# Kernel tuning notes

Measured on AMD Instinct MI355X. Metric: run time of the kernel, lower is better.

The kernel has to match this reference:

```python
import jax, jax.numpy as jnp
import numpy as np

B, S, D, H = 2, 2048, 1024, 16
DK = D // H


def setup_inputs() -> dict:
    key = jax.random.key(0)
    ks = jax.random.split(key, 11)
    sd = 1.0 / np.sqrt(D)  # torch Linear default init scale (uniform bound)
    def lin(k):
        kw, kb = jax.random.split(k)
        W = jax.random.uniform(kw, (D, D), jnp.float32, -sd, sd)
        b = jax.random.uniform(kb, (D,), jnp.float32, -sd, sd)
        return W, b
    Wq, bq = lin(ks[0]); Wk, bk = lin(ks[1]); Wv, bv = lin(ks[2]); Wo, bo = lin(ks[3])
    return {
        "Q": jax.random.normal(ks[4], (B, S, D), jnp.float32),
        "K": jax.random.normal(ks[5], (B, S, D), jnp.float32),
        "V": jax.random.normal(ks[6], (B, S, D), jnp.float32),
        "mask": jnp.ones((B, S), jnp.int32),
        "Wq": Wq, "bq": bq, "Wk": Wk, "bk": bk,
        "Wv": Wv, "bv": bv, "Wo": Wo, "bo": bo,
    }


def reference(Q, K, V, mask, Wq, bq, Wk, bk, Wv, bv, Wo, bo):
    b, s, _ = Q.shape
    # projections (torch Linear: x @ W.T + b), split heads -> [b, h, s, dk]
    def proj(x, W, bias):
        return (x @ W.T + bias).reshape(b, -1, H, DK).transpose(0, 2, 1, 3)
    q = proj(Q, Wq, bq)
    k = proj(K, Wk, bk)
    v = proj(V, Wv, bv)
    scores = jnp.einsum('bhqd,bhkd->bhqk', q, k) / jnp.sqrt(jnp.float32(DK))
    m = mask[:, None, None, :]  # [b,1,1,s_k]
    scores = jnp.where(m == 0, jnp.float32(-jnp.inf), scores)
    attn = jax.nn.softmax(scores, axis=-1)
    out = jnp.einsum('bhqk,bhkd->bhqd', attn, v)
    out = out.transpose(0, 2, 1, 3).reshape(b, s, H * DK)
    return out @ Wo.T + bo
```

## Files before the change

### kernel.cpp

```cpp
#include <hip/hip_runtime.h>
#include <stdint.h>

#define BB 2
#define HH 16
#define SS 2048
#define DKK 64
#define DD 1024
#define TT (BB * SS)

typedef __attribute__((ext_vector_type(8))) short bf16x8;
typedef __attribute__((ext_vector_type(4))) float f32x4;
typedef __attribute__((ext_vector_type(16))) float f32x16;

static __device__ __forceinline__ unsigned short f2bf(float f) {
  union { float f; uint32_t u; } c; c.f = f;
  return (unsigned short)((c.u + 0x7FFFu + ((c.u >> 16) & 1u)) >> 16);
}

static __device__ __forceinline__ f32x4 zero4() {
  f32x4 z; z[0] = 0.f; z[1] = 0.f; z[2] = 0.f; z[3] = 0.f; return z;
}
static __device__ __forceinline__ f32x16 zero16() {
  f32x16 z;
#pragma unroll
  for (int i = 0; i < 16; ++i) z[i] = 0.f;
  return z;
}

static __device__ __forceinline__ uint32_t cvt_pk_bf16(float lo, float hi) {
  uint32_t r;
  asm("v_cvt_pk_bf16_f32 %0, %1, %2" : "=v"(r) : "v"(lo), "v"(hi));
  return r;
}

static __device__ __forceinline__ uint32_t xswap_u32(uint32_t v) {
  return (uint32_t)__shfl_xor((int)v, 32);
}
static __device__ __forceinline__ float xhalf_sum(float x) {
  return x + __shfl_xor(x, 32);
}

static __device__ __forceinline__ void gload_lds16(const void* g, void* l) {
  __builtin_amdgcn_global_load_lds(
      (const __attribute__((address_space(1))) void*)g,
      (__attribute__((address_space(3))) void*)l, 16, 0, 0);
}

static __device__ __forceinline__ int swz(int row, int col) {
  return ((((col >> 3) ^ row) & 7) << 3) | (col & 7);
}

struct CvtArgs {
  const float* src[4];
  unsigned short* dst[4];
  int n4[4];
};

__global__ __launch_bounds__(256) void cvt_all(CvtArgs a) {
  const int id = blockIdx.y;
  const float4* s = (const float4*)a.src[id];
  ushort4* d = (ushort4*)a.dst[id];
  const int n4 = a.n4[id];
  for (int i = blockIdx.x * blockDim.x + threadIdx.x; i < n4;
       i += gridDim.x * blockDim.x) {
    float4 v = s[i];
    ushort4 o;
    o.x = f2bf(v.x); o.y = f2bf(v.y); o.z = f2bf(v.z); o.w = f2bf(v.w);
    d[i] = o;
  }
}

struct GemmJob {
  const void* A;
  const unsigned short* W;
  const float* bias;
  void* out;
  int mode;
  float scale;
};
struct GemmArgs { GemmJob job[3]; };

template <int BM, int NBUF, bool AFP32>
__global__ __launch_bounds__(256) void gemm_kernel(GemmArgs args) {
  constexpr int MI = BM / 32;
  __shared__ __align__(16) unsigned short As[NBUF][BM][64];
  __shared__ __align__(16) unsigned short Bs[NBUF][128][64];
  const GemmJob jb = args.job[blockIdx.z];
  const int tid = threadIdx.x;
  const int lane = tid & 63;
  const int wv = tid >> 6;
  const int fr = lane & 15, fq = lane >> 4;
  const int wr = (wv >> 1) * (BM / 2), wc = (wv & 1) * 64;

  const int nb = gridDim.x * gridDim.y;
  const int bid = blockIdx.y * gridDim.x + blockIdx.x;
  const int virt = (bid & 7) * (nb >> 3) + (bid >> 3);
  const int n0 = (virt & 7) * 128, m0 = (virt >> 3) * BM;

  const int lrow = lane >> 3;
  const int lchunk = (lane & 7) ^ lrow;
  const unsigned short* __restrict__ Ab = (const unsigned short*)jb.A;
  const float* __restrict__ A32 = (const float*)jb.A;
  const unsigned short* __restrict__ W = jb.W;

  f32x4 acc[MI][4];
#pragma unroll
  for (int i = 0; i < MI; ++i)
#pragma unroll
    for (int j = 0; j < 4; ++j) acc[i][j] = zero4();

  constexpr int SEGA_W = BM / 32;
  constexpr int NT = DD / 64;

#define GSTAGE(buf, k0)                                                      \
  {                                                                          \
    _Pragma("unroll") for (int i = 0; i < SEGA_W; ++i) {                     \
      const int seg = wv * SEGA_W + i;                                       \
      const int row = seg * 8 + lrow;                                        \
      if constexpr (AFP32) {                                                 \
        const float* sp = A32 + (size_t)(m0 + row) * DD + (k0) + lchunk * 8; \
        const float4 f0 = *(const float4*)sp;                                \
        const float4 f1 = *(const float4*)(sp + 4);                          \
        uint4 wdat;                                                          \
        wdat.x = cvt_pk_bf16(f0.x, f0.y);                                    \
        wdat.y = cvt_pk_bf16(f0.z, f0.w);                                    \
        wdat.z = cvt_pk_bf16(f1.x, f1.y);                                    \
        wdat.w = cvt_pk_bf16(f1.z, f1.w);                                    \
        *(uint4*)((char*)&As[buf][0][0] + seg * 1024 + lane * 16) = wdat;    \
      } else {                                                               \
        gload_lds16(Ab + (size_t)(m0 + row) * DD + (k0) + lchunk * 8,        \
                    (char*)&As[buf][0][0] + seg * 1024);                     \
      }                                                                      \
    }                                                                        \
    _Pragma("unroll") for (int i = 0; i < 4; ++i) {                          \
      const int seg = wv * 4 + i;                                            \
      const int row = seg * 8 + lrow;                                        \
      gload_lds16(W + (size_t)(n0 + row) * DD + (k0) + lchunk * 8,           \
                  (char*)&Bs[buf][0][0] + seg * 1024);                       \
    }                                                                        \
  }

  int cur = 0;
  GSTAGE(0, 0);

  for (int t = 0; t < NT; ++t) {
    __syncthreads();
    if (t + 1 < NT) GSTAGE(cur ^ 1, (t + 1) * 64);
#pragma unroll
    for (int kk = 0; kk < 2; ++kk) {
      bf16x8 af[MI], bfr[4];
#pragma unroll
      for (int i = 0; i < MI; ++i) {
        const int r = wr + i * 16 + fr;
        af[i] = *(const bf16x8*)&As[cur][r][swz(r, kk * 32 + fq * 8)];
      }
#pragma unroll
      for (int j = 0; j < 4; ++j) {
        const int r = wc + j * 16 + fr;
        bfr[j] = *(const bf16x8*)&Bs[cur][r][swz(r, kk * 32 + fq * 8)];
      }
      __builtin_amdgcn_s_setprio(1);
#pragma unroll
      for (int i = 0; i < MI; ++i)
#pragma unroll
        for (int j = 0; j < 4; ++j)
          acc[i][j] = __builtin_amdgcn_mfma_f32_16x16x32_bf16(af[i], bfr[j],
                                                              acc[i][j], 0, 0, 0);
      __builtin_amdgcn_s_setprio(0);
    }
    cur ^= 1;
  }
#undef GSTAGE

  const int mode = jb.mode;
  const float scale = jb.scale;
  if (mode == 1) {
    float* out = (float*)jb.out;
#pragma unroll
    for (int i = 0; i < MI; ++i)
#pragma unroll
      for (int j = 0; j < 4; ++j) {
        const int col = n0 + wc + j * 16 + fr;
        const float bv = jb.bias[col];
#pragma unroll
        for (int r = 0; r < 4; ++r) {
          const int row = m0 + wr + i * 16 + fq * 4 + r;
          out[(size_t)row * DD + col] = (acc[i][j][r] + bv) * scale;
        }
      }
  } else if (mode == 0) {
    unsigned short* out = (unsigned short*)jb.out;
#pragma unroll
    for (int i = 0; i < MI; ++i)
#pragma unroll
      for (int j = 0; j < 4; ++j) {
        const int col = n0 + wc + j * 16 + fr;
        const float bv = jb.bias[col];
        const int h = col >> 6, dk = col & 63;
#pragma unroll
        for (int r = 0; r < 4; ++r) {
          const int row = m0 + wr + i * 16 + fq * 4 + r;
          const int b = row >> 11, s = row & (SS - 1);
          out[(((size_t)(b * HH + h)) * SS + s) * DKK + dk] =
              f2bf((acc[i][j][r] + bv) * scale);
        }
      }
  } else {
    unsigned short* out = (unsigned short*)jb.out;
#pragma unroll
    for (int i = 0; i < MI; ++i)
#pragma unroll
      for (int j = 0; j < 4; ++j) {
        const int col = n0 + wc + j * 16 + fr;
        const float bv = jb.bias[col];
        const int h = col >> 6, dk = col & 63;
#pragma unroll
        for (int r = 0; r < 4; ++r) {
          const int row = m0 + wr + i * 16 + fq * 4 + r;
          const int b = row >> 11, s = row & (SS - 1);
          out[(((size_t)(b * HH + h)) * DKK + dk) * SS + s] =
              f2bf((acc[i][j][r] + bv) * scale);
        }
      }
  }
}

__global__ __launch_bounds__(512, 2) void attn_kernel(
    const unsigned short* __restrict__ qh, const unsigned short* __restrict__ kh,
    const unsigned short* __restrict__ vt, const int* __restrict__ maskp,
    unsigned short* __restrict__ ao) {
  __shared__ __align__(16) char smem[65536];

  const int tid = threadIdx.x;
  const int lane = tid & 63, wv = tid >> 6;
  const int lo = lane & 31, hi = lane >> 5;
  const int g = wv >> 2, qw = wv & 3;

  const int bid = blockIdx.x;
  const int virt = (bid & 7) * 32 + (bid >> 3);
  const int bh = virt >> 3, qblk = virt & 7;
  const int bB = bh >> 4, h = bh & 15;
  const int q0 = qblk * 256;
  const size_t base = (size_t)bh * SS * DKK;
  const size_t vbase = (size_t)bh * DKK * SS;

  const int lrow = lane >> 3;
  const int lchunk = (lane & 7) ^ lrow;
  const int srow = wv * 8 + lrow;

  bf16x8 aq[2][4];
#pragma unroll
  for (int st = 0; st < 2; ++st) {
    const int qrow = q0 + qw * 64 + st * 32 + lo;
#pragma unroll
    for (int tt = 0; tt < 4; ++tt)
      aq[st][tt] =
          *(const bf16x8*)(qh + base + (size_t)qrow * DKK + 16 * tt + hi * 8);
  }

  float lsum[2] = {0.f, 0.f};
  f32x16 o[2][2];
#pragma unroll
  for (int st = 0; st < 2; ++st) {
    o[st][0] = zero16();
    o[st][1] = zero16();
  }

  const int kvb = g * (SS / 2);
  constexpr int NTH = SS / 128;

  uint32_t okbits = 0;
  for (int t = 0; t < NTH; ++t) {
    const int mv = maskp[bB * SS + kvb + t * 64 + lane];
    okbits |= (__all(mv != 0)) ? (1u << t) : 0u;
  }

#define STAGE(d, t)                                                           \
  {                                                                           \
    const int ka = (t) * 64, kb2 = SS / 2 + (t) * 64;                         \
    gload_lds16(kh + base + (size_t)(ka + srow) * DKK + lchunk * 8,           \
                smem + ((d)) * 8192 + wv * 1024);                             \
    gload_lds16(vt + vbase + (size_t)srow * SS + ka + lchunk * 8,             \
                smem + 32768 + ((d)) * 8192 + wv * 1024);                     \
    gload_lds16(kh + base + (size_t)(kb2 + srow) * DKK + lchunk * 8,          \
                smem + (2 + (d)) * 8192 + wv * 1024);                         \
    gload_lds16(vt + vbase + (size_t)srow * SS + kb2 + lchunk * 8,            \
                smem + 32768 + (2 + (d)) * 8192 + wv * 1024);                 \
  }

  STAGE(0, 0);
  int cur = 0;

  for (int t = 0; t < NTH; ++t) {
    __syncthreads();
    if (t + 1 < NTH) STAGE(cur ^ 1, t + 1);
    const bool ok = (okbits >> t) & 1;

    const unsigned short* Ksb =
        (const unsigned short*)(smem + (g * 2 + cur) * 8192);
    const unsigned short* Vsb =
        (const unsigned short*)(smem + 32768 + (g * 2 + cur) * 8192);

    f32x16 sc[2][2];
#pragma unroll
    for (int st = 0; st < 2; ++st) { sc[st][0] = zero16(); sc[st][1] = zero16(); }
    __builtin_amdgcn_s_setprio(1);
#pragma unroll
    for (int tt = 0; tt < 4; ++tt) {
      bf16x8 k0 = *(const bf16x8*)&Ksb[lo * 64 + swz(lo, (hi + 2 * tt) * 8)];
      bf16x8 k1 =
          *(const bf16x8*)&Ksb[(32 + lo) * 64 + swz(32 + lo, (hi + 2 * tt) * 8)];
#pragma unroll
      for (int st = 0; st < 2; ++st) {
        sc[st][0] =
            __builtin_amdgcn_mfma_f32_32x32x16_bf16(k0, aq[st][tt], sc[st][0], 0, 0, 0);
        sc[st][1] =
            __builtin_amdgcn_mfma_f32_32x32x16_bf16(k1, aq[st][tt], sc[st][1], 0, 0, 0);
      }
    }
    __builtin_amdgcn_s_setprio(0);

    if (!ok) {
      const int mt = maskp[bB * SS + kvb + t * 64 + lane];
#pragma unroll
      for (int r = 0; r < 16; ++r) {
        const int kvi = (r & 3) + 8 * (r >> 2) + 4 * hi;
        const float a0 = (__shfl(mt, kvi) != 0) ? 0.f : -1e30f;
        const float a1 = (__shfl(mt, 32 + kvi) != 0) ? 0.f : -1e30f;
#pragma unroll
        for (int st = 0; st < 2; ++st) {
          sc[st][0][r] += a0;
          sc[st][1][r] += a1;
        }
      }
    }

    bf16x8 pb[2][4];
#pragma unroll
    for (int st = 0; st < 2; ++st) {
#pragma unroll
      for (int r = 0; r < 16; ++r) {
        sc[st][0][r] = __builtin_amdgcn_exp2f(sc[st][0][r]);
        sc[st][1][r] = __builtin_amdgcn_exp2f(sc[st][1][r]);
      }
      float t8[8];
#pragma unroll
      for (int i = 0; i < 8; ++i)
        t8[i] = (sc[st][0][2 * i] + sc[st][0][2 * i + 1]) +
                (sc[st][1][2 * i] + sc[st][1][2 * i + 1]);
      lsum[st] += ((t8[0] + t8[1]) + (t8[2] + t8[3])) +
                  ((t8[4] + t8[5]) + (t8[6] + t8[7]));

#pragma unroll
      for (int kb = 0; kb < 2; ++kb) {
#pragma unroll
        for (int tt = 0; tt < 2; ++tt) {
          const int b = tt * 8;
          uint32_t a0 = cvt_pk_bf16(sc[st][kb][b + 0], sc[st][kb][b + 1]);
          uint32_t a1 = cvt_pk_bf16(sc[st][kb][b + 2], sc[st][kb][b + 3]);
          uint32_t a2 = cvt_pk_bf16(sc[st][kb][b + 4], sc[st][kb][b + 5]);
          uint32_t a3 = cvt_pk_bf16(sc[st][kb][b + 6], sc[st][kb][b + 7]);
          const uint32_t e0 = xswap_u32(hi ? a0 : a2);
          const uint32_t e1 = xswap_u32(hi ? a1 : a3);
          union { uint32_t w[4]; bf16x8 v; } u;
          u.w[0] = hi ? e0 : a0;
          u.w[1] = hi ? e1 : a1;
          u.w[2] = hi ? a2 : e0;
          u.w[3] = hi ? a3 : e1;
          pb[st][kb * 2 + tt] = u.v;
        }
      }
    }

    __builtin_amdgcn_s_setprio(1);
#pragma unroll
    for (int tt = 0; tt < 4; ++tt) {
      bf16x8 v0 = *(const bf16x8*)&Vsb[lo * 64 + swz(lo, (hi + 2 * tt) * 8)];
      bf16x8 v1 =
          *(const bf16x8*)&Vsb[(32 + lo) * 64 + swz(32 + lo, (hi + 2 * tt) * 8)];
#pragma unroll
      for (int st = 0; st < 2; ++st) {
        o[st][0] = __builtin_amdgcn_mfma_f32_32x32x16_bf16(v0, pb[st][tt], o[st][0], 0, 0, 0);
        o[st][1] = __builtin_amdgcn_mfma_f32_32x32x16_bf16(v1, pb[st][tt], o[st][1], 0, 0, 0);
      }
    }
    __builtin_amdgcn_s_setprio(0);

    cur ^= 1;
  }
#undef STAGE

  lsum[0] = xhalf_sum(lsum[0]);
  lsum[1] = xhalf_sum(lsum[1]);

  float* mb = (float*)smem;
#pragma unroll
  for (int st = 0; st < 2; ++st) {
    const int rec = (qw * 64 + lane) * 33;
    __syncthreads();
    if (g == 1) {
      mb[rec] = lsum[st];
#pragma unroll
      for (int i = 0; i < 16; ++i) {
        mb[rec + 1 + i] = o[st][0][i];
        mb[rec + 17 + i] = o[st][1][i];
      }
    }
    __syncthreads();
    if (g == 0) {
      const float inv = 1.f / (lsum[st] + mb[rec]);
      const int token = bB * SS + q0 + qw * 64 + st * 32 + lo;
      unsigned short* aop = ao + (size_t)token * DD + h * DKK;
#pragma unroll
      for (int db = 0; db < 2; ++db) {
#pragma unroll
        for (int gq = 0; gq < 4; ++gq) {
          const int rb = rec + 1 + db * 16 + 4 * gq;
          float c0 = (o[st][db][4 * gq + 0] + mb[rb + 0]) * inv;
          float c1 = (o[st][db][4 * gq + 1] + mb[rb + 1]) * inv;
          float c2 = (o[st][db][4 * gq + 2] + mb[rb + 2]) * inv;
          float c3 = (o[st][db][4 * gq + 3] + mb[rb + 3]) * inv;
          uint2 w;
          w.x = cvt_pk_bf16(c0, c1);
          w.y = cvt_pk_bf16(c2, c3);
          *(uint2*)&aop[db * 32 + 8 * gq + 4 * hi] = w;
        }
      }
    }
  }
}

extern "C" void kernel_launch(void* const* d_in, const int* in_sizes, int n_in,
                              void* d_out, int out_size, void* d_ws, size_t ws_size,
                              hipStream_t stream) {
  const float* Q = (const float*)d_in[0];
  const float* K = (const float*)d_in[1];
  const float* V = (const float*)d_in[2];
  const int* mask = (const int*)d_in[3];
  const float* Wq = (const float*)d_in[4];
  const float* bq = (const float*)d_in[5];
  const float* Wk = (const float*)d_in[6];
  const float* bk = (const float*)d_in[7];
  const float* Wv = (const float*)d_in[8];
  const float* bv = (const float*)d_in[9];
  const float* Wo = (const float*)d_in[10];
  const float* bo = (const float*)d_in[11];

  char* ws = (char*)d_ws;
  const size_t SZ_X = (size_t)TT * DD * 2;
  const size_t SZ_W = (size_t)DD * DD * 2;
  unsigned short* Wqb = (unsigned short*)(ws + 0 * SZ_W);
  unsigned short* Wkb = (unsigned short*)(ws + 1 * SZ_W);
  unsigned short* Wvb = (unsigned short*)(ws + 2 * SZ_W);
  unsigned short* Wob = (unsigned short*)(ws + 3 * SZ_W);
  unsigned short* qh = (unsigned short*)(ws + 4 * SZ_W + 0 * SZ_X);
  unsigned short* kh = (unsigned short*)(ws + 4 * SZ_W + 1 * SZ_X);
  unsigned short* vt = (unsigned short*)(ws + 4 * SZ_W + 2 * SZ_X);
  unsigned short* ao = (unsigned short*)(ws + 4 * SZ_W + 3 * SZ_X);

  CvtArgs ca;
  ca.src[0] = Wq; ca.dst[0] = Wqb; ca.n4[0] = DD * DD / 4;
  ca.src[1] = Wk; ca.dst[1] = Wkb; ca.n4[1] = DD * DD / 4;
  ca.src[2] = Wv; ca.dst[2] = Wvb; ca.n4[2] = DD * DD / 4;
  ca.src[3] = Wo; ca.dst[3] = Wob; ca.n4[3] = DD * DD / 4;
  cvt_all<<<dim3(512, 4), 256, 0, stream>>>(ca);

  const float SCALE_Q = 0.125f * 1.44269504088896f;

  GemmArgs ga;
  ga.job[0] = {Q, Wqb, bq, qh, 0, SCALE_Q};
  ga.job[1] = {K, Wkb, bk, kh, 0, 1.0f};
  ga.job[2] = {V, Wvb, bv, vt, 2, 1.0f};
  gemm_kernel<64, 2, true><<<dim3(DD / 128, TT / 64, 3), 256, 0, stream>>>(ga);

  attn_kernel<<<dim3((TT / 256) * HH), 512, 0, stream>>>(qh, kh, vt, mask, ao);

  GemmArgs gf;
  gf.job[0] = {ao, Wob, bo, d_out, 1, 1.0f};
  gf.job[1] = gf.job[0];
  gf.job[2] = gf.job[0];
  gemm_kernel<64, 2, false><<<dim3(DD / 128, TT / 64, 1), 256, 0, stream>>>(gf);
}
```

Before: 113.0 us.

## Software-pipeline PV MFMA with next QK using triple-buffered V tiles

```diff
diff --git a/kernel.cpp b/kernel.cpp
--- a/kernel.cpp
+++ b/kernel.cpp
@@ -229,7 +229,7 @@
     const unsigned short* __restrict__ qh, const unsigned short* __restrict__ kh,
     const unsigned short* __restrict__ vt, const int* __restrict__ maskp,
     unsigned short* __restrict__ ao) {
-  __shared__ __align__(16) char smem[65536];
+  extern __shared__ __align__(16) char smem[];
 
   const int tid = threadIdx.x;
   const int lane = tid & 63, wv = tid >> 6;
@@ -275,31 +275,37 @@
     okbits |= (__all(mv != 0)) ? (1u << t) : 0u;
   }
 
-#define STAGE(d, t)                                                           \
+#define STAGE_K(sk, t)                                                        \
   {                                                                           \
     const int ka = (t) * 64, kb2 = SS / 2 + (t) * 64;                         \
     gload_lds16(kh + base + (size_t)(ka + srow) * DKK + lchunk * 8,           \
-                smem + ((d)) * 8192 + wv * 1024);                             \
+                smem + (0 * 2 + (sk)) * 8192 + wv * 1024);                    \
+    gload_lds16(kh + base + (size_t)(kb2 + srow) * DKK + lchunk * 8,          \
+                smem + (1 * 2 + (sk)) * 8192 + wv * 1024);                    \
+  }
+#define STAGE_V(sv, t)                                                        \
+  {                                                                           \
+    const int ka = (t) * 64, kb2 = SS / 2 + (t) * 64;                         \
     gload_lds16(vt + vbase + (size_t)srow * SS + ka + lchunk * 8,             \
-                smem + 32768 + ((d)) * 8192 + wv * 1024);                     \
-    gload_lds16(kh + base + (size_t)(kb2 + srow) * DKK + lchunk * 8,          \
-                smem + (2 + (d)) * 8192 + wv * 1024);                         \
+                smem + 32768 + (0 * 3 + (sv)) * 8192 + wv * 1024);            \
     gload_lds16(vt + vbase + (size_t)srow * SS + kb2 + lchunk * 8,            \
-                smem + 32768 + (2 + (d)) * 8192 + wv * 1024);                 \
-  }
-
-  STAGE(0, 0);
-  int cur = 0;
+                smem + 32768 + (1 * 3 + (sv)) * 8192 + wv * 1024);            \
+  }
+
+  STAGE_K(0, 0);
+  STAGE_V(0, 0);
+
+  bf16x8 pb[2][4];
 
   for (int t = 0; t < NTH; ++t) {
     __syncthreads();
-    if (t + 1 < NTH) STAGE(cur ^ 1, t + 1);
+    if (t + 1 < NTH) {
+      STAGE_K((t + 1) & 1, t + 1);
+      STAGE_V((t + 1) % 3, t + 1);
+    }
     const bool ok = (okbits >> t) & 1;
 
-    const unsigned short* Ksb =
-        (const unsigned short*)(smem + (g * 2 + cur) * 8192);
-    const unsigned short* Vsb =
-        (const unsigned short*)(smem + 32768 + (g * 2 + cur) * 8192);
+    const char* Ksb = smem + (g * 2 + (t & 1)) * 8192;
 
     f32x16 sc[2][2];
 #pragma unroll
@@ -307,9 +313,9 @@
     __builtin_amdgcn_s_setprio(1);
 #pragma unroll
     for (int tt = 0; tt < 4; ++tt) {
-      bf16x8 k0 = *(const bf16x8*)&Ksb[lo * 64 + swz(lo, (hi + 2 * tt) * 8)];
-      bf16x8 k1 =
-          *(const bf16x8*)&Ksb[(32 + lo) * 64 + swz(32 + lo, (hi + 2 * tt) * 8)];
+      bf16x8 k0 = *(const bf16x8*)(Ksb + (lo * 64 + swz(lo, (hi + 2 * tt) * 8)) * 2);
+      bf16x8 k1 = *(const bf16x8*)(Ksb + ((32 + lo) * 64 +
+                                          swz(32 + lo, (hi + 2 * tt) * 8)) * 2);
 #pragma unroll
       for (int st = 0; st < 2; ++st) {
         sc[st][0] =
@@ -318,6 +324,24 @@
             __builtin_amdgcn_mfma_f32_32x32x16_bf16(k1, aq[st][tt], sc[st][1], 0, 0, 0);
       }
     }
+
+    if (t > 0) {
+      const char* Vsb_p = smem + 32768 + (g * 3 + ((t + 2) % 3)) * 8192;
+#pragma unroll
+      for (int tt = 0; tt < 4; ++tt) {
+        bf16x8 v0 =
+            *(const bf16x8*)(Vsb_p + (lo * 64 + swz(lo, (hi + 2 * tt) * 8)) * 2);
+        bf16x8 v1 = *(const bf16x8*)(Vsb_p + ((32 + lo) * 64 +
+                                              swz(32 + lo, (hi + 2 * tt) * 8)) * 2);
+#pragma unroll
+        for (int st = 0; st < 2; ++st) {
+          o[st][0] = __builtin_amdgcn_mfma_f32_32x32x16_bf16(v0, pb[st][tt],
+                                                             o[st][0], 0, 0, 0);
+          o[st][1] = __builtin_amdgcn_mfma_f32_32x32x16_bf16(v1, pb[st][tt],
+                                                             o[st][1], 0, 0, 0);
+        }
+      }
+    }
     __builtin_amdgcn_s_setprio(0);
 
     if (!ok) {
@@ -335,7 +359,6 @@
       }
     }
 
-    bf16x8 pb[2][4];
 #pragma unroll
     for (int st = 0; st < 2; ++st) {
 #pragma unroll
@@ -371,13 +394,17 @@
         }
       }
     }
-
+  }
+
+  {
+    const char* Vsb = smem + 32768 + (g * 3 + ((NTH - 1) % 3)) * 8192;
     __builtin_amdgcn_s_setprio(1);
 #pragma unroll
     for (int tt = 0; tt < 4; ++tt) {
-      bf16x8 v0 = *(const bf16x8*)&Vsb[lo * 64 + swz(lo, (hi + 2 * tt) * 8)];
-      bf16x8 v1 =
-          *(const bf16x8*)&Vsb[(32 + lo) * 64 + swz(32 + lo, (hi + 2 * tt) * 8)];
+      bf16x8 v0 =
+          *(const bf16x8*)(Vsb + (lo * 64 + swz(lo, (hi + 2 * tt) * 8)) * 2);
+      bf16x8 v1 = *(const bf16x8*)(Vsb + ((32 + lo) * 64 +
+                                          swz(32 + lo, (hi + 2 * tt) * 8)) * 2);
 #pragma unroll
       for (int st = 0; st < 2; ++st) {
         o[st][0] = __builtin_amdgcn_mfma_f32_32x32x16_bf16(v0, pb[st][tt], o[st][0], 0, 0, 0);
@@ -385,10 +412,9 @@
       }
     }
     __builtin_amdgcn_s_setprio(0);
-
-    cur ^= 1;
-  }
-#undef STAGE
+  }
+#undef STAGE_K
+#undef STAGE_V
 
   lsum[0] = xhalf_sum(lsum[0]);
   lsum[1] = xhalf_sum(lsum[1]);
@@ -473,7 +499,7 @@
   ga.job[2] = {V, Wvb, bv, vt, 2, 1.0f};
   gemm_kernel<64, 2, true><<<dim3(DD / 128, TT / 64, 3), 256, 0, stream>>>(ga);
 
-  attn_kernel<<<dim3((TT / 256) * HH), 512, 0, stream>>>(qh, kh, vt, mask, ao);
+  attn_kernel<<<dim3((TT / 256) * HH), 512, 81920, stream>>>(qh, kh, vt, mask, ao);
 
   GemmArgs gf;
   gf.job[0] = {ao, Wob, bo, d_out, 1, 1.0f};
```

New measurement: 115.5 us. 1.02x slower.
